# Kernel optimization log

Measured on AMD Instinct MI355X. Metric: run time of the kernel, lower is better.

Reference implementation:

```python
import jax, jax.numpy as jnp
import numpy as np

SUBSET_CHANNELS = 128


def setup_inputs() -> dict:
    key = jax.random.key(0)
    k_in, k_q, k_k, k_v = jax.random.split(key, 4)
    B, S, C, D = 8, 2048, 1024, SUBSET_CHANNELS
    scale = 1.0 / np.sqrt(C)  # ~ default torch Linear init scale
    return {
        "input": jax.random.normal(k_in, (B, S, C), dtype=jnp.float32),
        "Wq": jax.random.normal(k_q, (C, D), dtype=jnp.float32) * scale,
        "Wk": jax.random.normal(k_k, (C, D), dtype=jnp.float32) * scale,
        "Wv": jax.random.normal(k_v, (C, D), dtype=jnp.float32) * scale,
    }


def reference(input, Wq, Wk, Wv):
    # Projections (bias=False): [B,S,C] @ [C,D] -> [B,S,D]
    Q = input @ Wq
    K = input @ Wk
    V = input @ Wv
    D = Wq.shape[1]
    # scores[b, i, j] = Q[b,i,:] . K[b,j,:], scaled by sqrt(subset_channels)
    scores = jnp.einsum("bqd,bkd->bqk", Q, K) / jnp.sqrt(jnp.asarray(D, Q.dtype))
    # NOTE: original applies softmax over dim=1 (the QUERY axis), non-standard.
    att = jax.nn.softmax(scores, axis=1)
    # output[b, i, :] = sum_j att[b,i,j] * V[b,j,:]
    return jnp.einsum("bqk,bkd->bqd", att, V)
```

## Files before the change

kernel.cpp:

```cpp
#include <hip/hip_runtime.h>
#include <hip/hip_bf16.h>

typedef __bf16 bf16_t;
typedef bf16_t bf16x4 __attribute__((ext_vector_type(4)));
typedef bf16_t bf16x8 __attribute__((ext_vector_type(8)));
typedef float f32x4 __attribute__((ext_vector_type(4)));
typedef __attribute__((address_space(1))) const unsigned int gu32_t;
typedef __attribute__((address_space(3))) unsigned int lu32_t;

#define MFMA(a, b, c) __builtin_amdgcn_mfma_f32_16x16x32_bf16(a, b, c, 0, 0, 0)

constexpr int B = 8, S = 2048, C = 1024, D = 128;
constexpr float C2 = 0.12751744f;


__global__ __launch_bounds__(256) void k_wt(const float* Wq, const float* Wk, const float* Wv, bf16_t* Wf) {
    int ct = blockIdx.x, w = blockIdx.y;
    const float* src = (w == 0) ? Wq : ((w == 1) ? Wk : Wv);
    __shared__ bf16_t tile[16][132];
    int t = threadIdx.x;
    int cr = t >> 4, dq = t & 15;
    const float* p = src + (size_t)(ct * 16 + cr) * D + dq * 8;
    f32x4 v0 = *(const f32x4*)p;
    f32x4 v1 = *(const f32x4*)(p + 4);
#pragma unroll
    for (int q = 0; q < 4; ++q) { tile[cr][dq * 8 + q] = (bf16_t)v0[q]; tile[cr][dq * 8 + 4 + q] = (bf16_t)v1[q]; }
    __syncthreads();
    int n = t >> 1, g = t & 1;
    bf16x8 o;
#pragma unroll
    for (int cc = 0; cc < 8; ++cc) o[cc] = tile[g * 8 + cc][n];
    int c8 = ct * 2 + g;
    int nblk = w * 8 + (n >> 4);
    size_t a = ((size_t)(nblk * 32 + (c8 >> 2)) * 64 + (c8 & 3) * 16 + (n & 15)) * 8;
    *(bf16x8*)(Wf + a) = o;
}

__global__ __launch_bounds__(512, 4) void k_qkv(const float* X, const bf16_t* Wf,
                                                bf16_t* Qf, bf16_t* Kf, float* Vf,
                                                float* Out) {
    __shared__ __align__(16) bf16_t xs[2][2048];
    int mt = blockIdx.x;
    int t = threadIdx.x;
    int lane = t & 63, wid = t >> 6;
    int lr = lane & 15, lg = lane >> 4;
    int rw = mt * 32;
    int xrow = t >> 4, xk = t & 15;
    const float* xsrc = X + (size_t)(rw + xrow) * C + xk * 4;
    int xwi = ((xk >> 1) * 32 + xrow) * 8 + (xk & 1) * 4;

    {
        f32x4* O4 = (f32x4*)Out;
        f32x4 z = {};
        int u = mt * 512 + t;
        O4[u] = z;
        O4[u + 262144] = z;
    }

    f32x4 acc[2][3] = {};

    auto wfrag = [&](int nf, int kk32) {
        return *(const bf16x8*)(Wf + ((size_t)((wid * 3 + nf) * 32 + kk32) * 64 + lane) * 8);
    };
    auto xld = [&](int s) { return *(const f32x4*)(xsrc + s * 64); };
    auto xst = [&](int bufi, f32x4 xv) {
        bf16x4 c;
#pragma unroll
        for (int q = 0; q < 4; ++q) c[q] = (bf16_t)xv[q];
        *(bf16x4*)&xs[bufi][xwi] = c;
    };

    bf16x8 wCur[2][3];
#pragma unroll
    for (int kh = 0; kh < 2; ++kh)
#pragma unroll
        for (int nf = 0; nf < 3; ++nf) wCur[kh][nf] = wfrag(nf, kh);
    xst(0, xld(0));
    f32x4 xP1 = xld(1), xP2 = xld(2);
    __syncthreads();

#pragma unroll
    for (int tt = 0; tt < 16; ++tt) {
        int buf = tt & 1;
        bf16x8 wNxt[2][3];
        if (tt < 15) {
#pragma unroll
            for (int kh = 0; kh < 2; ++kh)
#pragma unroll
                for (int nf = 0; nf < 3; ++nf) wNxt[kh][nf] = wfrag(nf, (tt + 1) * 2 + kh);
        }
        f32x4 xNext = {};
        if (tt < 13) xNext = xld(tt + 3);
#pragma unroll
        for (int kh = 0; kh < 2; ++kh) {
            bf16x8 a0 = *(bf16x8*)&xs[buf][((kh * 4 + lg) * 32 + lr) * 8];
            bf16x8 a1 = *(bf16x8*)&xs[buf][((kh * 4 + lg) * 32 + 16 + lr) * 8];
#pragma unroll
            for (int nf = 0; nf < 3; ++nf) {
                acc[0][nf] = MFMA(a0, wCur[kh][nf], acc[0][nf]);
                acc[1][nf] = MFMA(a1, wCur[kh][nf], acc[1][nf]);
            }
        }
        if (tt < 15) {
            xst(buf ^ 1, xP1);
#pragma unroll
            for (int kh = 0; kh < 2; ++kh)
#pragma unroll
                for (int nf = 0; nf < 3; ++nf) wCur[kh][nf] = wNxt[kh][nf];
        }
        xP1 = xP2; xP2 = xNext;
        __syncthreads();
    }
#pragma unroll
    for (int mi = 0; mi < 2; ++mi)
#pragma unroll
        for (int nf = 0; nf < 3; ++nf) {
            int n = wid * 48 + nf * 16 + lr;
            int sel = (wid * 48 + nf * 16) >> 7;
            int nn = n & 127;
#pragma unroll
            for (int r = 0; r < 4; ++r) {
                int m = rw + mi * 16 + lg * 4 + r;
                float v = acc[mi][nf][r];
                if (sel == 2) {
                    Vf[(size_t)m * D + nn] = v;
                } else {
                    bf16_t* dst = (sel == 0) ? Qf : Kf;
                    size_t a = ((size_t)((m >> 4) * 4 + (nn >> 5)) * 64 + ((nn >> 3) & 3) * 16 + (m & 15)) * 8 + (nn & 7);
                    dst[a] = (bf16_t)v;
                }
            }
        }
}

__global__ __launch_bounds__(512, 4) void k_sum(const bf16_t* Qf, const bf16_t* Kf,
                                                const float* Vf, bf16_t* Vt2) {
    int l = blockIdx.x;
    int b = l & 7, jt = l >> 3;
    int j0 = jt * 32;
    int t = threadIdx.x;
    int lane = t & 63, wid = t >> 6;
    __shared__ __align__(16) bf16_t qs[2][16384];
    bf16_t* vtile = qs[0];
    float* lsum = (float*)(qs[0] + 6144);
    float* linv = (float*)(qs[0] + 6656);

    bf16x8 kf[2][4];
    int jblkg = (b * S + j0) >> 4;
#pragma unroll
    for (int jF = 0; jF < 2; ++jF)
#pragma unroll
        for (int kk = 0; kk < 4; ++kk)
            kf[jF][kk] = *(const bf16x8*)(Kf + ((size_t)((jblkg + jF) * 4 + kk) * 64 + lane) * 8);

    const bf16_t* qsrc = Qf + (size_t)(b * S) * 128;
    auto stageQ = [&](int bufi, int i0) {
#pragma unroll
        for (int i = 0; i < 4; ++i)
            __builtin_amdgcn_global_load_lds(
                (gu32_t*)(qsrc + (size_t)i0 * 128 + wid * 2048 + i * 512 + lane * 8),
                (lu32_t*)&qs[bufi][wid * 2048 + i * 512], 16, 0, 0);
    };

    float ls0 = 0.f, ls1 = 0.f;
    stageQ(0, 0);
    __syncthreads();
    for (int tt = 0; tt < 16; ++tt) {
        int buf = tt & 1;
        if (tt < 15) stageQ(buf ^ 1, (tt + 1) * 128);
        bf16x8 qa[4];
#pragma unroll
        for (int kk = 0; kk < 4; ++kk)
            qa[kk] = *(const bf16x8*)&qs[buf][(wid * 4 + kk) * 512 + lane * 8];
        f32x4 s0 = {}, s1 = {};
#pragma unroll
        for (int kk = 0; kk < 4; ++kk) {
            s0 = MFMA(qa[kk], kf[0][kk], s0);
            s1 = MFMA(qa[kk], kf[1][kk], s1);
        }
#pragma unroll
        for (int r = 0; r < 4; ++r) { ls0 += exp2f(s0[r] * C2); ls1 += exp2f(s1[r] * C2); }
        __syncthreads();
    }
    {
        float v0 = ls0 + __shfl_xor(ls0, 16); v0 += __shfl_xor(v0, 32);
        float v1 = ls1 + __shfl_xor(ls1, 16); v1 += __shfl_xor(v1, 32);
        if (lane < 16) { lsum[wid * 32 + lane] = v0; lsum[wid * 32 + 16 + lane] = v1; }
    }
    __syncthreads();
    if (t < 32) {
        float ss = 0.f;
#pragma unroll
        for (int w = 0; w < 8; ++w) ss += lsum[w * 32 + t];
        linv[t] = 1.0f / ss;
    }
    __syncthreads();
#pragma unroll
    for (int p = 0; p < 2; ++p) {
        int u = p * 512 + t;
        int jj = u & 31, dq = u >> 5;
        f32x4 v = *(const f32x4*)(Vf + (size_t)(b * S + j0 + jj) * D + dq * 4);
        float inv = linv[jj];
#pragma unroll
        for (int q = 0; q < 4; ++q)
            vtile[(dq * 4 + q) * 40 + jj] = (bf16_t)(v[q] * inv);
    }
    __syncthreads();
    {
        int d = t >> 2, jg = t & 3;
        bf16x8 row = *(const bf16x8*)&vtile[d * 40 + jg * 8];
        size_t j32g = (size_t)b * 64 + jt;
        size_t a = ((j32g * 8 + (d >> 4)) * 64 + jg * 16 + (d & 15)) * 8;
        *(bf16x8*)(Vt2 + a) = row;
    }
}

__global__ __launch_bounds__(512, 4) void k_out(const bf16_t* Qf, const bf16_t* Kf,
                                                const bf16_t* Vt2, float* Out) {
    int l = blockIdx.x;
    int b = l & 7, it = (l >> 3) & 31, jh = l >> 8;
    int ibase = it * 64;
    int t = threadIdx.x;
    int lane = t & 63, wid = t >> 6;
    int lr = lane & 15, lg = lane >> 4;
    int ig = wid >> 1, jq = wid & 1;
    __shared__ __align__(16) bf16_t pool[37888];
    bf16_t* klds = pool;
    bf16_t* vlds = pool + 16384;
    bf16_t* pl = pool + 32768 + wid * 640;

    bf16x8 qf[4];
    int iblk = (b * S + ibase + ig * 16) >> 4;
#pragma unroll
    for (int kk = 0; kk < 4; ++kk)
        qf[kk] = *(const bf16x8*)(Qf + ((size_t)(iblk * 4 + kk) * 64 + lane) * 8);

    f32x4 acc[8] = {};
    const bf16_t* kbase = Kf + (size_t)(b * S + jh * 1024) * 128 + wid * 1024 + lane * 8;
    const bf16_t* vbase = Vt2 + (size_t)(b * 64 + jh * 32) * 4096 + wid * 1024 + lane * 8;

    auto stageKV = [&](int bufi, int tt) {
        const bf16_t* gk = kbase + (size_t)tt * 8192;
        __builtin_amdgcn_global_load_lds((gu32_t*)gk, (lu32_t*)&klds[bufi * 8192 + wid * 1024], 16, 0, 0);
        __builtin_amdgcn_global_load_lds((gu32_t*)(gk + 512), (lu32_t*)&klds[bufi * 8192 + wid * 1024 + 512], 16, 0, 0);
        const bf16_t* gv = vbase + (size_t)tt * 8192;
        __builtin_amdgcn_global_load_lds((gu32_t*)gv, (lu32_t*)&vlds[bufi * 8192 + wid * 1024], 16, 0, 0);
        __builtin_amdgcn_global_load_lds((gu32_t*)(gv + 512), (lu32_t*)&vlds[bufi * 8192 + wid * 1024 + 512], 16, 0, 0);
    };
    stageKV(0, 0);
    __syncthreads();

    for (int tt = 0; tt < 16; ++tt) {
        int buf = tt & 1;
        if (tt < 15) stageKV(buf ^ 1, tt + 1);
#pragma unroll
        for (int jF = 0; jF < 2; ++jF) {
            const bf16_t* kl = &klds[buf * 8192 + ((jq * 2 + jF) * 4) * 512 + lane * 8];
            f32x4 s = {};
            s = MFMA(*(const bf16x8*)(kl), qf[0], s);
            s = MFMA(*(const bf16x8*)(kl + 512), qf[1], s);
            s = MFMA(*(const bf16x8*)(kl + 1024), qf[2], s);
            s = MFMA(*(const bf16x8*)(kl + 1536), qf[3], s);
            bf16x4 pv;
#pragma unroll
            for (int r = 0; r < 4; ++r) pv[r] = (bf16_t)exp2f(s[r] * C2);
            *(bf16x4*)&pl[lr * 40 + jF * 16 + lg * 4] = pv;
        }
        bf16x8 pa = *(const bf16x8*)&pl[lr * 40 + lg * 8];
        const bf16_t* vl = &vlds[buf * 8192 + jq * 4096 + lane * 8];
        __builtin_amdgcn_s_setprio(1);
#pragma unroll
        for (int dc = 0; dc < 8; ++dc)
            acc[dc] = MFMA(pa, *(const bf16x8*)(vl + dc * 512), acc[dc]);
        __builtin_amdgcn_s_setprio(0);
        __syncthreads();
    }

    float* R = (float*)pool + ig * 2048;
    if (jq == 1) {
#pragma unroll
        for (int dc = 0; dc < 8; ++dc)
#pragma unroll
            for (int r = 0; r < 4; ++r)
                R[(lg * 4 + r) * 128 + dc * 16 + lr] = acc[dc][r];
    }
    __syncthreads();
    if (jq == 0) {
#pragma unroll
        for (int dc = 0; dc < 8; ++dc)
#pragma unroll
            for (int r = 0; r < 4; ++r)
                atomicAdd(&Out[(size_t)(b * S + ibase + ig * 16 + lg * 4 + r) * 128 + dc * 16 + lr],
                          acc[dc][r] + R[(lg * 4 + r) * 128 + dc * 16 + lr]);
    }
}

extern "C" void kernel_launch(void* const* d_in, const int* in_sizes, int n_in,
                              void* d_out, int out_size, void* d_ws, size_t ws_size,
                              hipStream_t stream) {
    const float* X  = (const float*)d_in[0];
    const float* Wq = (const float*)d_in[1];
    const float* Wk = (const float*)d_in[2];
    const float* Wv = (const float*)d_in[3];
    char* ws = (char*)d_ws;
    bf16_t* Wf  = (bf16_t*)(ws);
    bf16_t* Qf  = (bf16_t*)(ws + (1ull << 20));
    bf16_t* Kf  = (bf16_t*)(ws + (5ull << 20));
    float*  Vf  = (float*)(ws + (9ull << 20));
    bf16_t* Vt2 = (bf16_t*)(ws + (17ull << 20));
    float* Out = (float*)d_out;

    k_wt<<<dim3(64, 3), dim3(256), 0, stream>>>(Wq, Wk, Wv, Wf);
    k_qkv<<<dim3(512), dim3(512), 0, stream>>>(X, Wf, Qf, Kf, Vf, Out);
    k_sum<<<dim3(512), dim3(512), 0, stream>>>(Qf, Kf, Vf, Vt2);
    k_out<<<dim3(512), dim3(512), 0, stream>>>(Qf, Kf, Vt2, Out);
}
```

Baseline: 86.58 us.

## Stage whole X tile in LDS once and read Q directly from global

New measurement: 87.37 us. Within noise of the previous version (+0.9%).

```diff
diff --git a/kernel.cpp b/kernel.cpp
--- a/kernel.cpp
+++ b/kernel.cpp
@@ -39,15 +39,12 @@
 __global__ __launch_bounds__(512, 4) void k_qkv(const float* X, const bf16_t* Wf,
                                                 bf16_t* Qf, bf16_t* Kf, float* Vf,
                                                 float* Out) {
-    __shared__ __align__(16) bf16_t xs[2][2048];
+    __shared__ __align__(16) bf16_t xfr[64 * 512];
     int mt = blockIdx.x;
     int t = threadIdx.x;
     int lane = t & 63, wid = t >> 6;
     int lr = lane & 15, lg = lane >> 4;
     int rw = mt * 32;
-    int xrow = t >> 4, xk = t & 15;
-    const float* xsrc = X + (size_t)(rw + xrow) * C + xk * 4;
-    int xwi = ((xk >> 1) * 32 + xrow) * 8 + (xk & 1) * 4;
 
     {
         f32x4* O4 = (f32x4*)Out;
@@ -57,60 +54,39 @@
         O4[u + 262144] = z;
     }
 
+    f32x4 xa[8], xb[8];
+#pragma unroll
+    for (int p = 0; p < 8; ++p) {
+        int fi = p * 8 + wid;
+        int m = rw + (fi >> 5) * 16 + lr;
+        int c = (fi & 31) * 32 + lg * 8;
+        const float* px = X + (size_t)m * C + c;
+        xa[p] = *(const f32x4*)px;
+        xb[p] = *(const f32x4*)(px + 4);
+    }
+#pragma unroll
+    for (int p = 0; p < 8; ++p) {
+        bf16x8 o;
+#pragma unroll
+        for (int q = 0; q < 4; ++q) { o[q] = (bf16_t)xa[p][q]; o[4 + q] = (bf16_t)xb[p][q]; }
+        *(bf16x8*)&xfr[(size_t)(p * 8 + wid) * 512 + lane * 8] = o;
+    }
+    __syncthreads();
+
     f32x4 acc[2][3] = {};
-
-    auto wfrag = [&](int nf, int kk32) {
-        return *(const bf16x8*)(Wf + ((size_t)((wid * 3 + nf) * 32 + kk32) * 64 + lane) * 8);
-    };
-    auto xld = [&](int s) { return *(const f32x4*)(xsrc + s * 64); };
-    auto xst = [&](int bufi, f32x4 xv) {
-        bf16x4 c;
-#pragma unroll
-        for (int q = 0; q < 4; ++q) c[q] = (bf16_t)xv[q];
-        *(bf16x4*)&xs[bufi][xwi] = c;
-    };
-
-    bf16x8 wCur[2][3];
-#pragma unroll
-    for (int kh = 0; kh < 2; ++kh)
-#pragma unroll
-        for (int nf = 0; nf < 3; ++nf) wCur[kh][nf] = wfrag(nf, kh);
-    xst(0, xld(0));
-    f32x4 xP1 = xld(1), xP2 = xld(2);
-    __syncthreads();
-
-#pragma unroll
-    for (int tt = 0; tt < 16; ++tt) {
-        int buf = tt & 1;
-        bf16x8 wNxt[2][3];
-        if (tt < 15) {
-#pragma unroll
-            for (int kh = 0; kh < 2; ++kh)
-#pragma unroll
-                for (int nf = 0; nf < 3; ++nf) wNxt[kh][nf] = wfrag(nf, (tt + 1) * 2 + kh);
-        }
-        f32x4 xNext = {};
-        if (tt < 13) xNext = xld(tt + 3);
-#pragma unroll
-        for (int kh = 0; kh < 2; ++kh) {
-            bf16x8 a0 = *(bf16x8*)&xs[buf][((kh * 4 + lg) * 32 + lr) * 8];
-            bf16x8 a1 = *(bf16x8*)&xs[buf][((kh * 4 + lg) * 32 + 16 + lr) * 8];
-#pragma unroll
-            for (int nf = 0; nf < 3; ++nf) {
-                acc[0][nf] = MFMA(a0, wCur[kh][nf], acc[0][nf]);
-                acc[1][nf] = MFMA(a1, wCur[kh][nf], acc[1][nf]);
-            }
-        }
-        if (tt < 15) {
-            xst(buf ^ 1, xP1);
-#pragma unroll
-            for (int kh = 0; kh < 2; ++kh)
-#pragma unroll
-                for (int nf = 0; nf < 3; ++nf) wCur[kh][nf] = wNxt[kh][nf];
-        }
-        xP1 = xP2; xP2 = xNext;
-        __syncthreads();
-    }
+    const bf16_t* wbase = Wf + (size_t)(wid * 3) * 32 * 512;
+#pragma unroll 8
+    for (int kk = 0; kk < 32; ++kk) {
+        bf16x8 a0 = *(const bf16x8*)&xfr[(size_t)kk * 512 + lane * 8];
+        bf16x8 a1 = *(const bf16x8*)&xfr[(size_t)(32 + kk) * 512 + lane * 8];
+#pragma unroll
+        for (int nf = 0; nf < 3; ++nf) {
+            bf16x8 w = *(const bf16x8*)(wbase + ((size_t)(nf * 32 + kk)) * 512 + lane * 8);
+            acc[0][nf] = MFMA(a0, w, acc[0][nf]);
+            acc[1][nf] = MFMA(a1, w, acc[1][nf]);
+        }
+    }
+
 #pragma unroll
     for (int mi = 0; mi < 2; ++mi)
 #pragma unroll
@@ -140,10 +116,9 @@
     int j0 = jt * 32;
     int t = threadIdx.x;
     int lane = t & 63, wid = t >> 6;
-    __shared__ __align__(16) bf16_t qs[2][16384];
-    bf16_t* vtile = qs[0];
-    float* lsum = (float*)(qs[0] + 6144);
-    float* linv = (float*)(qs[0] + 6656);
+    __shared__ __align__(16) bf16_t vtile[128 * 40];
+    __shared__ float lsum[256];
+    __shared__ float linv[32];
 
     bf16x8 kf[2][4];
     int jblkg = (b * S + j0) >> 4;
@@ -153,25 +128,14 @@
         for (int kk = 0; kk < 4; ++kk)
             kf[jF][kk] = *(const bf16x8*)(Kf + ((size_t)((jblkg + jF) * 4 + kk) * 64 + lane) * 8);
 
-    const bf16_t* qsrc = Qf + (size_t)(b * S) * 128;
-    auto stageQ = [&](int bufi, int i0) {
-#pragma unroll
-        for (int i = 0; i < 4; ++i)
-            __builtin_amdgcn_global_load_lds(
-                (gu32_t*)(qsrc + (size_t)i0 * 128 + wid * 2048 + i * 512 + lane * 8),
-                (lu32_t*)&qs[bufi][wid * 2048 + i * 512], 16, 0, 0);
-    };
-
     float ls0 = 0.f, ls1 = 0.f;
-    stageQ(0, 0);
-    __syncthreads();
+#pragma unroll 4
     for (int tt = 0; tt < 16; ++tt) {
-        int buf = tt & 1;
-        if (tt < 15) stageQ(buf ^ 1, (tt + 1) * 128);
+        int iblk = (b * S + wid * 256 + tt * 16) >> 4;
         bf16x8 qa[4];
 #pragma unroll
         for (int kk = 0; kk < 4; ++kk)
-            qa[kk] = *(const bf16x8*)&qs[buf][(wid * 4 + kk) * 512 + lane * 8];
+            qa[kk] = *(const bf16x8*)(Qf + ((size_t)(iblk * 4 + kk) * 64 + lane) * 8);
         f32x4 s0 = {}, s1 = {};
 #pragma unroll
         for (int kk = 0; kk < 4; ++kk) {
@@ -180,7 +144,6 @@
         }
 #pragma unroll
         for (int r = 0; r < 4; ++r) { ls0 += exp2f(s0[r] * C2); ls1 += exp2f(s1[r] * C2); }
-        __syncthreads();
     }
     {
         float v0 = ls0 + __shfl_xor(ls0, 16); v0 += __shfl_xor(v0, 32);
```
